# Performance work log

Measured on AMD Instinct MI355X. Metric: run time of the kernel, lower is better.

## Reference

```python
import jax, jax.numpy as jnp
import numpy as np

NORM_EPS = 1e-6
QK_SCALE = 1.0 / 128.0  # 1/d_head (muP)
ROTARY_BASE = 10000
INFTY_APPROX = 1e30

B, T, M, H, D = 2, 2048, 1024, 8, 128


def _rmsnorm(x, eps=NORM_EPS):
    # normalize over the last (head) dim; no learned gains (norm_gains=False)
    ms = jnp.mean(jnp.square(x), axis=-1, keepdims=True)
    return x / jnp.sqrt(ms + eps)


def _rope(x, base=ROTARY_BASE):
    # x: [b, h, t, d]; rotate (even-half, odd-half) pairs as in the source
    length, width = x.shape[-2], x.shape[-1]
    half = width // 2
    pos = jnp.arange(length, dtype=x.dtype)[:, None]            # [t, 1]
    freqs = jnp.power(jnp.asarray(base, x.dtype), -jnp.arange(half, dtype=x.dtype) / half)[None, :]
    rad = pos * freqs                                            # [t, half]
    cos = jnp.cos(rad)[None, None]
    sin = jnp.sin(rad)[None, None]
    even, odd = jnp.split(x, 2, axis=-1)
    return jnp.concatenate([even * cos - odd * sin, even * sin + odd * cos], axis=-1)


def setup_inputs() -> dict:
    key = jax.random.key(0)
    ks = jax.random.split(key, 5)
    std = M ** -0.5
    return {
        "x": jax.random.normal(ks[0], (B, T, M), jnp.float32),
        "wq": jax.random.normal(ks[1], (M, H, D), jnp.float32) * std,
        "wk": jax.random.normal(ks[2], (M, H, D), jnp.float32) * std,
        "wv": jax.random.normal(ks[3], (M, H, D), jnp.float32) * std,
        "wo": jax.random.normal(ks[4], (H, D, M), jnp.float32) * std,
    }


def reference(x, wq, wk, wv, wo):
    # projections: [b, h, t, d]
    q = jnp.einsum('bim,mhd->bhid', x, wq)
    k = jnp.einsum('bim,mhd->bhid', x, wk)
    v = jnp.einsum('bim,mhd->bhid', x, wv)
    # qk RMSNorm (norm_gains=False)
    q = _rmsnorm(q)
    k = _rmsnorm(k)
    # inline RoPE
    q = _rope(q)
    k = _rope(k)
    # scaled scores: mult applied to both q and k (mult^2 = qk_scale)
    mult = jnp.asarray(QK_SCALE ** 0.5, q.dtype)
    s = jnp.einsum('bhid,bhjd->bhij', q * mult, k * mult)
    # causal mask: subtract large constant where i < j
    t = s.shape[-1]
    mask = (jnp.arange(t)[:, None] < jnp.arange(t)[None, :]).astype(s.dtype)
    s = s - jnp.asarray(INFTY_APPROX, s.dtype) * mask[None, None]
    p = jax.nn.softmax(s, axis=-1)
    o = jnp.einsum('bhij,bhjd->bhid', p, v)
    return jnp.einsum('bhid,hdm->bim', o, wo)
```

## Files before the change

### kernel.cpp

```cpp
#include <hip/hip_runtime.h>
#include <hip/hip_bf16.h>
#include <math.h>

#define B_  2
#define T_  2048
#define M_  1024
#define H_  8
#define D_  128
#define NROW (B_ * T_)
#define HD  (H_ * D_)

#define NORM_EPS 1e-6f
#define QK_MULT  0.08838834764831845f
#define LN_BASE_64 0.14391156510f

typedef short bf16x8  __attribute__((ext_vector_type(8)));
typedef float f32x4   __attribute__((ext_vector_type(4)));
typedef float f32x16  __attribute__((ext_vector_type(16)));
typedef unsigned int uint32x2 __attribute__((ext_vector_type(2)));

static __device__ __forceinline__ unsigned short f2bf(float f) {
    union { __hip_bfloat16 h; unsigned short u; } cv;
    cv.h = __float2bfloat16(f);
    return cv.u;
}
static __device__ __forceinline__ unsigned int pk2bf(float a, float b) {
    return ((unsigned int)f2bf(b) << 16) | f2bf(a);
}

static __device__ __forceinline__ void gload_lds16(const unsigned short* g,
                                                   unsigned short* l) {
    __builtin_amdgcn_global_load_lds(
        (const __attribute__((address_space(1))) void*)g,
        (__attribute__((address_space(3))) void*)l, 16, 0, 0);
}

__global__ __launch_bounds__(256) void prep(const float* __restrict__ x,
                                            const float* __restrict__ w0,
                                            const float* __restrict__ w1,
                                            const float* __restrict__ w2,
                                            const float* __restrict__ w3,
                                            unsigned short* __restrict__ xb,
                                            unsigned short* __restrict__ wqkvT,
                                            unsigned short* __restrict__ woT,
                                            int* __restrict__ ctr)
{
    __shared__ float t[32][33];
    const int z = blockIdx.z;
    if (z == 4) {
        if (blockIdx.x == 0 && blockIdx.y == 0 && threadIdx.x < 8)
            ctr[threadIdx.x] = 0;
        const size_t base = ((size_t)blockIdx.y * 32 + blockIdx.x) * 4096;
        #pragma unroll
        for (int it = 0; it < 4; ++it) {
            const size_t i = base + it * 1024 + threadIdx.x * 4;
            const float4 v = *(const float4*)(x + i);
            ushort4 o;
            o.x = f2bf(v.x); o.y = f2bf(v.y); o.z = f2bf(v.z); o.w = f2bf(v.w);
            *(ushort4*)(xb + i) = o;
        }
        return;
    }
    const float* in = z == 0 ? w0 : (z == 1 ? w1 : (z == 2 ? w2 : w3));
    unsigned short* out = z < 3 ? (wqkvT + (size_t)z * 1024 * 1024) : woT;

    const int tx = threadIdx.x & 31;
    const int ty = threadIdx.x >> 5;
    const int n0 = blockIdx.x * 32;
    const int k0 = blockIdx.y * 32;
    #pragma unroll
    for (int r = 0; r < 4; ++r)
        t[ty + r * 8][tx] = in[(size_t)(k0 + ty + r * 8) * 1024 + n0 + tx];
    __syncthreads();
    #pragma unroll
    for (int r = 0; r < 4; ++r)
        out[(size_t)(n0 + ty + r * 8) * 1024 + k0 + tx] = f2bf(t[tx][ty + r * 8]);
}

__global__ __launch_bounds__(256) void gemm_qkv(const unsigned short* __restrict__ A,
                                                const unsigned short* __restrict__ Bt,
                                                unsigned short* __restrict__ oq,
                                                unsigned short* __restrict__ ok,
                                                unsigned short* __restrict__ vt)
{
    __shared__ __align__(16) unsigned short smem[17408];
    #define AsQ(buf) (smem + (buf) * 4096)
    #define BsQ(buf) (smem + 8192 + (buf) * 4096)

    const int tid  = threadIdx.x;
    const int lane = tid & 63;
    const int w    = tid >> 6;
    const int g    = lane >> 4;
    const int lc   = lane & 15;

    const int m0 = blockIdx.y * 128;
    const int n0 = blockIdx.x * 128;

    const unsigned short* aBase = A  + (size_t)m0 * 1024;
    const unsigned short* bBase = Bt + (size_t)n0 * 1024;

    int dstOff[2];
    size_t srcOff[2];
    #pragma unroll
    for (int it = 0; it < 2; ++it) {
        const int u  = tid + it * 256;
        const int r2 = u >> 2;
        const int sg = (u & 3) ^ (r2 & 3);
        dstOff[it] = u * 8;
        srcOff[it] = (size_t)r2 * 1024 + sg * 8;
    }

    f32x4 acc[2][8];
    #pragma unroll
    for (int i = 0; i < 2; ++i)
        #pragma unroll
        for (int j = 0; j < 8; ++j)
            acc[i][j] = (f32x4){0.f, 0.f, 0.f, 0.f};

    #pragma unroll
    for (int it = 0; it < 2; ++it) {
        gload_lds16(aBase + srcOff[it], AsQ(0) + dstOff[it]);
        gload_lds16(bBase + srcOff[it], BsQ(0) + dstOff[it]);
    }

    for (int kt = 0; kt < 32; ++kt) {
        const int cur = kt & 1;
        __syncthreads();

        if (kt < 31) {
            const int k0n = (kt + 1) * 32;
            #pragma unroll
            for (int it = 0; it < 2; ++it) {
                gload_lds16(aBase + srcOff[it] + k0n, AsQ(cur ^ 1) + dstOff[it]);
                gload_lds16(bBase + srcOff[it] + k0n, BsQ(cur ^ 1) + dstOff[it]);
            }
        }

        const int sw = (g ^ (lc & 3)) << 3;
        bf16x8 af[2], bfr[8];
        #pragma unroll
        for (int i = 0; i < 2; ++i)
            af[i] = *(const bf16x8*)&AsQ(cur)[(w * 32 + i * 16 + lc) * 32 + sw];
        #pragma unroll
        for (int j = 0; j < 8; ++j)
            bfr[j] = *(const bf16x8*)&BsQ(cur)[(j * 16 + lc) * 32 + sw];

        #pragma unroll
        for (int i = 0; i < 2; ++i)
            #pragma unroll
            for (int j = 0; j < 8; ++j)
                acc[i][j] = __builtin_amdgcn_mfma_f32_16x16x32_bf16(af[i], bfr[j], acc[i][j], 0, 0, 0);
    }

    const int which = n0 >> 10;
    const int ncol0 = n0 & 1023;
    if (which < 2) {
        unsigned short* outp = which == 0 ? oq : ok;
        float freq[4];
        #pragma unroll
        for (int j = 0; j < 4; ++j)
            freq[j] = __expf(-(float)(j * 16 + lc) * LN_BASE_64);

        #pragma unroll
        for (int i = 0; i < 2; ++i)
            #pragma unroll
            for (int r = 0; r < 4; ++r) {
                float s = 0.f;
                #pragma unroll
                for (int j = 0; j < 8; ++j) s += acc[i][j][r] * acc[i][j][r];
                #pragma unroll
                for (int off = 1; off < 16; off <<= 1) s += __shfl_xor(s, off);
                const float rms = rsqrtf(s * (1.0f / 128.0f) + NORM_EPS) * QK_MULT;

                const int trow = m0 + w * 32 + i * 16 + g * 4 + r;
                const float tpos = (float)(trow & (T_ - 1));
                unsigned short* op = outp + (size_t)trow * 1024 + ncol0;
                #pragma unroll
                for (int j = 0; j < 4; ++j) {
                    float sn, cs;
                    __sincosf(tpos * freq[j], &sn, &cs);
                    const float e = acc[i][j][r] * rms;
                    const float o = acc[i][j + 4][r] * rms;
                    op[j * 16 + lc]      = f2bf(e * cs - o * sn);
                    op[j * 16 + lc + 64] = f2bf(e * sn + o * cs);
                }
            }
    } else {
        const int b2 = m0 >> 11;
        const int hh = ncol0 >> 7;
        const int PAD = 136;
        __syncthreads();
        #pragma unroll
        for (int i = 0; i < 2; ++i) {
            const int t0 = w * 32 + i * 16 + g * 4;
            #pragma unroll
            for (int j = 0; j < 8; ++j) {
                uint2 val;
                val.x = pk2bf(acc[i][j][0], acc[i][j][1]);
                val.y = pk2bf(acc[i][j][2], acc[i][j][3]);
                *(uint2*)&smem[(j * 16 + lc) * PAD + t0] = val;
            }
        }
        __syncthreads();
        const int row  = tid >> 1;
        const int half = tid & 1;
        const unsigned short* src = &smem[row * PAD + half * 64];
        unsigned short* dst = vt + ((size_t)(b2 * 8 + hh) * 128 + row) * T_
                                 + (m0 & 2047) + half * 64;
        #pragma unroll
        for (int it2 = 0; it2 < 8; ++it2)
            *(uint4*)(dst + it2 * 8) = *(const uint4*)(src + it2 * 8);
    }
    #undef AsQ
    #undef BsQ
}

__global__ __launch_bounds__(256) void gemm_out(const unsigned short* __restrict__ A,
                                                const unsigned short* __restrict__ Bt,
                                                float* __restrict__ cf)
{
    __shared__ unsigned short As[2][128 * 64];
    __shared__ unsigned short Bs[2][64 * 64];

    const int tid  = threadIdx.x;
    const int lane = tid & 63;
    const int w    = tid >> 6;
    const int g    = lane >> 4;
    const int lc   = lane & 15;
    const int wm   = w >> 1;
    const int wn   = w & 1;

    const int m0 = blockIdx.y * 128;
    const int n0 = blockIdx.x * 64;

    const unsigned short* aBase = A  + (size_t)m0 * 1024;
    const unsigned short* bBase = Bt + (size_t)n0 * 1024;

    int dstA[4], dstB[2];
    size_t srcA[4], srcB[2];
    #pragma unroll
    for (int it = 0; it < 4; ++it) {
        const int u  = tid + it * 256;
        const int r2 = u >> 3;
        const int sg = (u & 7) ^ (r2 & 7);
        dstA[it] = u * 8;
        srcA[it] = (size_t)r2 * 1024 + sg * 8;
    }
    #pragma unroll
    for (int it = 0; it < 2; ++it) {
        const int u  = tid + it * 256;
        const int r2 = u >> 3;
        const int sg = (u & 7) ^ (r2 & 7);
        dstB[it] = u * 8;
        srcB[it] = (size_t)r2 * 1024 + sg * 8;
    }

    f32x4 acc[4][2];
    #pragma unroll
    for (int i = 0; i < 4; ++i)
        #pragma unroll
        for (int j = 0; j < 2; ++j)
            acc[i][j] = (f32x4){0.f, 0.f, 0.f, 0.f};

    #pragma unroll
    for (int it = 0; it < 4; ++it)
        gload_lds16(aBase + srcA[it], &As[0][dstA[it]]);
    #pragma unroll
    for (int it = 0; it < 2; ++it)
        gload_lds16(bBase + srcB[it], &Bs[0][dstB[it]]);

    for (int kt = 0; kt < 16; ++kt) {
        const int cur = kt & 1;
        __syncthreads();

        if (kt < 15) {
            const int k0n = (kt + 1) * 64;
            #pragma unroll
            for (int it = 0; it < 4; ++it)
                gload_lds16(aBase + srcA[it] + k0n, &As[cur ^ 1][dstA[it]]);
            #pragma unroll
            for (int it = 0; it < 2; ++it)
                gload_lds16(bBase + srcB[it] + k0n, &Bs[cur ^ 1][dstB[it]]);
        }

        #pragma unroll
        for (int dc = 0; dc < 2; ++dc) {
            const int sw = ((dc * 4 + g) ^ (lc & 7)) << 3;
            bf16x8 af[4], bfr[2];
            #pragma unroll
            for (int i = 0; i < 4; ++i)
                af[i] = *(const bf16x8*)&As[cur][(wm * 64 + i * 16 + lc) * 64 + sw];
            #pragma unroll
            for (int j = 0; j < 2; ++j)
                bfr[j] = *(const bf16x8*)&Bs[cur][(wn * 32 + j * 16 + lc) * 64 + sw];

            #pragma unroll
            for (int i = 0; i < 4; ++i)
                #pragma unroll
                for (int j = 0; j < 2; ++j)
                    acc[i][j] = __builtin_amdgcn_mfma_f32_16x16x32_bf16(af[i], bfr[j], acc[i][j], 0, 0, 0);
        }
    }

    #pragma unroll
    for (int i = 0; i < 4; ++i) {
        const int mrow = m0 + wm * 64 + i * 16 + g * 4;
        #pragma unroll
        for (int j = 0; j < 2; ++j) {
            const int nc = n0 + wn * 32 + j * 16 + lc;
            #pragma unroll
            for (int r = 0; r < 4; ++r)
                cf[(size_t)(mrow + r) * 1024 + nc] = acc[i][j][r];
        }
    }
}

__global__ __launch_bounds__(256) void flash_attn(const unsigned short* __restrict__ qb,
                                                  const unsigned short* __restrict__ kb,
                                                  const unsigned short* __restrict__ vt,
                                                  unsigned short* __restrict__ o,
                                                  int* __restrict__ ctr)
{
    __shared__ __align__(16) unsigned short smem[2 * 64 * 128 + 2 * 128 * 64 + 128];
    __shared__ int unitLds;
    unsigned short* KsB = smem;
    unsigned short* VsB = smem + 2 * 64 * 128;
    float* lscr = (float*)(smem + 2 * 64 * 128 + 2 * 128 * 64);
    float* scr  = (float*)smem;

    const int tid  = threadIdx.x;
    const int lane = tid & 63;
    const int w    = tid >> 6;
    const int wj   = w >> 1;
    const int wq2  = w & 1;
    const int qcol = lane & 31;
    const int hi   = lane >> 5;

    const int p = blockIdx.x & 7;

    int mI[4];
    size_t srcKoff[4], srcVoff[4];
    #pragma unroll
    for (int it = 0; it < 4; ++it) {
        const int m = (w * 4 + it) * 64 + lane;
        mI[it] = m;
        const int jK = m >> 4, cK = (m & 15) ^ (jK & 15);
        srcKoff[it] = (size_t)jK * 1024 + cK * 8;
        const int dV = m >> 3, cV = (m & 7) ^ (dV & 7);
        srcVoff[it] = (size_t)dV * T_ + cV * 8;
    }

    for (;;) {
        if (tid == 0) unitLds = atomicAdd(&ctr[p], 1);
        __syncthreads();
        const int u = unitLds;
        if (u >= 64) break;
        const int qt = 31 - (u >> 1);
        const int bh = p + 8 * (u & 1);
        const int q0 = qt * 64;
        const int h  = bh & (H_ - 1);
        const int b  = bh >> 3;

        const size_t bhbase  = (size_t)b * T_ * HD + (size_t)h * 128;
        const size_t bhvbase = (size_t)bh * 128 * T_;
        const unsigned short* kgb = kb + bhbase;
        const unsigned short* vgb = vt + bhvbase;

        bf16x8 qf[8];
        {
            const unsigned short* qp = qb + bhbase + (size_t)(q0 + wq2 * 32 + qcol) * 1024 + hi * 8;
            #pragma unroll
            for (int ks = 0; ks < 8; ++ks)
                qf[ks] = *(const bf16x8*)(qp + ks * 16);
        }

        float lsum = 0.f;
        f32x16 otacc[4];
        #pragma unroll
        for (int dch = 0; dch < 4; ++dch)
            #pragma unroll
            for (int r = 0; r < 16; ++r) otacc[dch][r] = 0.f;

        #pragma unroll
        for (int it = 0; it < 4; ++it) {
            gload_lds16(kgb + srcKoff[it], &KsB[mI[it] * 8]);
            gload_lds16(vgb + srcVoff[it], &VsB[mI[it] * 8]);
        }

        for (int jt = 0; jt <= qt; ++jt) {
            const int cur = jt & 1;
            unsigned short* Ks = KsB + cur * (64 * 128);
            unsigned short* Vs = VsB + cur * (128 * 64);
            __syncthreads();

            if (jt < qt) {
                const size_t j0n = (size_t)(jt + 1) * 64;
                unsigned short* Kn = KsB + (cur ^ 1) * (64 * 128);
                unsigned short* Vn = VsB + (cur ^ 1) * (128 * 64);
                #pragma unroll
                for (int it = 0; it < 4; ++it) {
                    gload_lds16(kgb + j0n * 1024 + srcKoff[it], &Kn[mI[it] * 8]);
                    gload_lds16(vgb + j0n + srcVoff[it], &Vn[mI[it] * 8]);
                }
            }

            const bool dead = (jt == qt) && (wj > wq2);
            if (!dead) {
                const int jrow = wj * 32 + qcol;

                bf16x8 kf[8], vf[8];
                #pragma unroll
                for (int ks = 0; ks < 8; ++ks) {
                    const int c = ks * 2 + hi;
                    kf[ks] = *(const bf16x8*)&Ks[(jrow * 16 + (c ^ (lane & 15))) * 8];
                }
                #pragma unroll
                for (int ks2 = 0; ks2 < 2; ++ks2)
                    #pragma unroll
                    for (int dch = 0; dch < 4; ++dch) {
                        const int c = wj * 4 + ks2 * 2 + hi;
                        const int drow = dch * 32 + qcol;
                        vf[ks2 * 4 + dch] = *(const bf16x8*)&Vs[(drow * 8 + (c ^ (lane & 7))) * 8];
                    }

                f32x16 sacc0, sacc1;
                #pragma unroll
                for (int r = 0; r < 16; ++r) { sacc0[r] = 0.f; sacc1[r] = 0.f; }
                __builtin_amdgcn_s_setprio(1);
                #pragma unroll
                for (int ks = 0; ks < 8; ks += 2) {
                    sacc0 = __builtin_amdgcn_mfma_f32_32x32x16_bf16(kf[ks], qf[ks], sacc0, 0, 0, 0);
                    sacc1 = __builtin_amdgcn_mfma_f32_32x32x16_bf16(kf[ks + 1], qf[ks + 1], sacc1, 0, 0, 0);
                }
                __builtin_amdgcn_s_setprio(0);
                f32x16 sacc = sacc0 + sacc1;

                if (jt == qt && wj == wq2) {
                    #pragma unroll
                    for (int r = 0; r < 16; ++r) {
                        const int jl = (r & 3) + 8 * (r >> 2) + 4 * hi;
                        if (qcol < jl) sacc[r] = -1e30f;
                    }
                }

                unsigned int dw[8];
                #pragma unroll
                for (int m2 = 0; m2 < 8; ++m2) {
                    const float p0 = __expf(sacc[2 * m2]);
                    const float p1 = __expf(sacc[2 * m2 + 1]);
                    lsum += p0 + p1;
                    dw[m2] = pk2bf(p0, p1);
                }

                __builtin_amdgcn_s_setprio(1);
                #pragma unroll
                for (int ks2 = 0; ks2 < 2; ++ks2) {
                    const uint32x2 s02 = __builtin_amdgcn_permlane32_swap(
                        dw[4 * ks2 + 0], dw[4 * ks2 + 2], 0, 0);
                    const uint32x2 s13 = __builtin_amdgcn_permlane32_swap(
                        dw[4 * ks2 + 1], dw[4 * ks2 + 3], 0, 0);
                    union { unsigned int u2[4]; bf16x8 v; } pf;
                    pf.u2[0] = s02[0];
                    pf.u2[1] = s13[0];
                    pf.u2[2] = s02[1];
                    pf.u2[3] = s13[1];
                    #pragma unroll
                    for (int dch = 0; dch < 4; ++dch)
                        otacc[dch] = __builtin_amdgcn_mfma_f32_32x32x16_bf16(vf[ks2 * 4 + dch], pf.v, otacc[dch], 0, 0, 0);
                }
                __builtin_amdgcn_s_setprio(0);
            }
        }

        lsum += __shfl_xor(lsum, 32);
        __syncthreads();

        if (wj == 1) {
            float* s0 = scr + (size_t)(wq2 * 32 + qcol) * 129;
            #pragma unroll
            for (int dch = 0; dch < 4; ++dch)
                #pragma unroll
                for (int r = 0; r < 16; ++r)
                    s0[dch * 32 + (r & 3) + 8 * (r >> 2) + 4 * hi] = otacc[dch][r];
            if (hi == 0) lscr[wq2 * 32 + qcol] = lsum;
        }
        __syncthreads();
        if (wj == 0) {
            const float l = lsum + lscr[wq2 * 32 + qcol];
            const float inv = 1.0f / l;
            const float* s0 = scr + (size_t)(wq2 * 32 + qcol) * 129;
            unsigned short* op = o + bhbase + (size_t)(q0 + wq2 * 32 + qcol) * 1024;
            #pragma unroll
            for (int dch = 0; dch < 4; ++dch) {
                #pragma unroll
                for (int k4 = 0; k4 < 4; ++k4) {
                    const int d0 = dch * 32 + 8 * k4 + 4 * hi;
                    const float f0 = (otacc[dch][4 * k4 + 0] + s0[d0 + 0]) * inv;
                    const float f1 = (otacc[dch][4 * k4 + 1] + s0[d0 + 1]) * inv;
                    const float f2 = (otacc[dch][4 * k4 + 2] + s0[d0 + 2]) * inv;
                    const float f3 = (otacc[dch][4 * k4 + 3] + s0[d0 + 3]) * inv;
                    uint2 val;
                    val.x = pk2bf(f0, f1);
                    val.y = pk2bf(f2, f3);
                    *(uint2*)(op + d0) = val;
                }
            }
        }
        __syncthreads();
    }
}

extern "C" void kernel_launch(void* const* d_in, const int* in_sizes, int n_in,
                              void* d_out, int out_size, void* d_ws, size_t ws_size,
                              hipStream_t stream)
{
    const float* x  = (const float*)d_in[0];
    const float* wq = (const float*)d_in[1];
    const float* wk = (const float*)d_in[2];
    const float* wv = (const float*)d_in[3];
    const float* wo = (const float*)d_in[4];
    float* out = (float*)d_out;

    const size_t SZ = (size_t)NROW * HD;
    unsigned short* qb    = (unsigned short*)d_ws;
    unsigned short* kb    = qb + SZ;
    unsigned short* vt    = kb + SZ;
    unsigned short* ob    = vt + SZ;
    unsigned short* xb    = ob + SZ;
    unsigned short* wqkvT = xb + SZ;
    unsigned short* woT   = wqkvT + 3 * 1024 * 1024;
    int* ctr = (int*)out;

    prep<<<dim3(32, 32, 5), 256, 0, stream>>>(x, wq, wk, wv, wo, xb, wqkvT, woT, ctr);

    gemm_qkv<<<dim3(24, 32), 256, 0, stream>>>(xb, wqkvT, qb, kb, vt);

    flash_attn<<<dim3(512), 256, 0, stream>>>(qb, kb, vt, ob, ctr);

    gemm_out<<<dim3(16, 32), 256, 0, stream>>>(ob, woT, out);
}
```

Baseline: 193.1 us.

## Split long causal query tiles across two blocks and merge partial outputs

Replaces the persistent atomic work-queue scheduling in flash attention with a static 48x16 grid. The 16 longest query tiles per head get two blocks, each covering half of the KV range. The first finisher writes unnormalized fp32 partial output and row sums to a scratch buffer (reusing the xb region), and the second spins on a per-tile counter, adds the partials and normalizes. This is meant to shorten the critical path of the longest causal tiles and improve load balance, at the cost of extra global traffic, a spin-wait that assumes both halves are co-resident, and more blocks overall.

```diff
diff --git a/kernel.cpp b/kernel.cpp
--- a/kernel.cpp
+++ b/kernel.cpp
@@ -43,13 +43,13 @@
                                             unsigned short* __restrict__ xb,
                                             unsigned short* __restrict__ wqkvT,
                                             unsigned short* __restrict__ woT,
-                                            int* __restrict__ ctr)
+                                            int* __restrict__ tctr)
 {
     __shared__ float t[32][33];
     const int z = blockIdx.z;
     if (z == 4) {
-        if (blockIdx.x == 0 && blockIdx.y == 0 && threadIdx.x < 8)
-            ctr[threadIdx.x] = 0;
+        if (blockIdx.x == 0 && blockIdx.y == 0)
+            tctr[threadIdx.x] = 0;
         const size_t base = ((size_t)blockIdx.y * 32 + blockIdx.x) * 4096;
         #pragma unroll
         for (int it = 0; it < 4; ++it) {
@@ -319,10 +319,12 @@
                                                   const unsigned short* __restrict__ kb,
                                                   const unsigned short* __restrict__ vt,
                                                   unsigned short* __restrict__ o,
-                                                  int* __restrict__ ctr)
+                                                  float* __restrict__ opart,
+                                                  float* __restrict__ lpart,
+                                                  int* __restrict__ tctr)
 {
     __shared__ __align__(16) unsigned short smem[2 * 64 * 128 + 2 * 128 * 64 + 128];
-    __shared__ int unitLds;
+    __shared__ int oldLds;
     unsigned short* KsB = smem;
     unsigned short* VsB = smem + 2 * 64 * 128;
     float* lscr = (float*)(smem + 2 * 64 * 128 + 2 * 128 * 64);
@@ -336,7 +338,25 @@
     const int qcol = lane & 31;
     const int hi   = lane >> 5;
 
-    const int p = blockIdx.x & 7;
+    const int x  = blockIdx.x;
+    const int bh = blockIdx.y;
+    int qt, jlo, jhi;
+    bool split;
+    if (x < 32) {
+        qt = 31 - (x & 15);
+        const int hsp = (qt + 2) >> 1;
+        split = true;
+        if (x < 16) { jlo = 0;   jhi = hsp - 1; }
+        else        { jlo = hsp; jhi = qt; }
+    } else {
+        qt = 47 - x; jlo = 0; jhi = qt; split = false;
+    }
+    const int q0 = qt * 64;
+    const int h  = bh & (H_ - 1);
+    const int b  = bh >> 3;
+
+    const size_t bhbase  = (size_t)b * T_ * HD + (size_t)h * 128;
+    const size_t bhvbase = (size_t)bh * 128 * T_;
 
     int mI[4];
     size_t srcKoff[4], srcVoff[4];
@@ -349,147 +369,141 @@
         const int dV = m >> 3, cV = (m & 7) ^ (dV & 7);
         srcVoff[it] = (size_t)dV * T_ + cV * 8;
     }
-
-    for (;;) {
-        if (tid == 0) unitLds = atomicAdd(&ctr[p], 1);
+    const unsigned short* kgb = kb + bhbase;
+    const unsigned short* vgb = vt + bhvbase;
+
+    bf16x8 qf[8];
+    {
+        const unsigned short* qp = qb + bhbase + (size_t)(q0 + wq2 * 32 + qcol) * 1024 + hi * 8;
+        #pragma unroll
+        for (int ks = 0; ks < 8; ++ks)
+            qf[ks] = *(const bf16x8*)(qp + ks * 16);
+    }
+
+    float lsum = 0.f;
+    f32x16 otacc[4];
+    #pragma unroll
+    for (int dch = 0; dch < 4; ++dch)
+        #pragma unroll
+        for (int r = 0; r < 16; ++r) otacc[dch][r] = 0.f;
+
+    {
+        const size_t j00 = (size_t)jlo * 64;
+        #pragma unroll
+        for (int it = 0; it < 4; ++it) {
+            gload_lds16(kgb + j00 * 1024 + srcKoff[it], &KsB[mI[it] * 8]);
+            gload_lds16(vgb + j00 + srcVoff[it], &VsB[mI[it] * 8]);
+        }
+    }
+
+    for (int jt = jlo; jt <= jhi; ++jt) {
+        const int cur = (jt - jlo) & 1;
+        unsigned short* Ks = KsB + cur * (64 * 128);
+        unsigned short* Vs = VsB + cur * (128 * 64);
         __syncthreads();
-        const int u = unitLds;
-        if (u >= 64) break;
-        const int qt = 31 - (u >> 1);
-        const int bh = p + 8 * (u & 1);
-        const int q0 = qt * 64;
-        const int h  = bh & (H_ - 1);
-        const int b  = bh >> 3;
-
-        const size_t bhbase  = (size_t)b * T_ * HD + (size_t)h * 128;
-        const size_t bhvbase = (size_t)bh * 128 * T_;
-        const unsigned short* kgb = kb + bhbase;
-        const unsigned short* vgb = vt + bhvbase;
-
-        bf16x8 qf[8];
-        {
-            const unsigned short* qp = qb + bhbase + (size_t)(q0 + wq2 * 32 + qcol) * 1024 + hi * 8;
-            #pragma unroll
-            for (int ks = 0; ks < 8; ++ks)
-                qf[ks] = *(const bf16x8*)(qp + ks * 16);
-        }
-
-        float lsum = 0.f;
-        f32x16 otacc[4];
+
+        if (jt < jhi) {
+            const size_t j0n = (size_t)(jt + 1) * 64;
+            unsigned short* Kn = KsB + (cur ^ 1) * (64 * 128);
+            unsigned short* Vn = VsB + (cur ^ 1) * (128 * 64);
+            #pragma unroll
+            for (int it = 0; it < 4; ++it) {
+                gload_lds16(kgb + j0n * 1024 + srcKoff[it], &Kn[mI[it] * 8]);
+                gload_lds16(vgb + j0n + srcVoff[it], &Vn[mI[it] * 8]);
+            }
+        }
+
+        const bool dead = (jt == qt) && (wj > wq2);
+        if (!dead) {
+            const int jrow = wj * 32 + qcol;
+
+            bf16x8 kf[8], vf[8];
+            #pragma unroll
+            for (int ks = 0; ks < 8; ++ks) {
+                const int c = ks * 2 + hi;
+                kf[ks] = *(const bf16x8*)&Ks[(jrow * 16 + (c ^ (lane & 15))) * 8];
+            }
+            #pragma unroll
+            for (int ks2 = 0; ks2 < 2; ++ks2)
+                #pragma unroll
+                for (int dch = 0; dch < 4; ++dch) {
+                    const int c = wj * 4 + ks2 * 2 + hi;
+                    const int drow = dch * 32 + qcol;
+                    vf[ks2 * 4 + dch] = *(const bf16x8*)&Vs[(drow * 8 + (c ^ (lane & 7))) * 8];
+                }
+
+            f32x16 sacc0, sacc1;
+            #pragma unroll
+            for (int r = 0; r < 16; ++r) { sacc0[r] = 0.f; sacc1[r] = 0.f; }
+            __builtin_amdgcn_s_setprio(1);
+            #pragma unroll
+            for (int ks = 0; ks < 8; ks += 2) {
+                sacc0 = __builtin_amdgcn_mfma_f32_32x32x16_bf16(kf[ks], qf[ks], sacc0, 0, 0, 0);
+                sacc1 = __builtin_amdgcn_mfma_f32_32x32x16_bf16(kf[ks + 1], qf[ks + 1], sacc1, 0, 0, 0);
+            }
+            __builtin_amdgcn_s_setprio(0);
+            f32x16 sacc = sacc0 + sacc1;
+
+            if (jt == qt && wj == wq2) {
+                #pragma unroll
+                for (int r = 0; r < 16; ++r) {
+                    const int jl = (r & 3) + 8 * (r >> 2) + 4 * hi;
+                    if (qcol < jl) sacc[r] = -1e30f;
+                }
+            }
+
+            unsigned int dw[8];
+            #pragma unroll
+            for (int m2 = 0; m2 < 8; ++m2) {
+                const float p0 = __expf(sacc[2 * m2]);
+                const float p1 = __expf(sacc[2 * m2 + 1]);
+                lsum += p0 + p1;
+                dw[m2] = pk2bf(p0, p1);
+            }
+
+            __builtin_amdgcn_s_setprio(1);
+            #pragma unroll
+            for (int ks2 = 0; ks2 < 2; ++ks2) {
+                const uint32x2 s02 = __builtin_amdgcn_permlane32_swap(
+                    dw[4 * ks2 + 0], dw[4 * ks2 + 2], 0, 0);
+                const uint32x2 s13 = __builtin_amdgcn_permlane32_swap(
+                    dw[4 * ks2 + 1], dw[4 * ks2 + 3], 0, 0);
+                union { unsigned int u2[4]; bf16x8 v; } pf;
+                pf.u2[0] = s02[0];
+                pf.u2[1] = s13[0];
+                pf.u2[2] = s02[1];
+                pf.u2[3] = s13[1];
+                #pragma unroll
+                for (int dch = 0; dch < 4; ++dch)
+                    otacc[dch] = __builtin_amdgcn_mfma_f32_32x32x16_bf16(vf[ks2 * 4 + dch], pf.v, otacc[dch], 0, 0, 0);
+            }
+            __builtin_amdgcn_s_setprio(0);
+        }
+    }
+
+    lsum += __shfl_xor(lsum, 32);
+    __syncthreads();
+
+    if (wj == 1) {
+        float* s0 = scr + (size_t)(wq2 * 32 + qcol) * 129;
         #pragma unroll
         for (int dch = 0; dch < 4; ++dch)
             #pragma unroll
-            for (int r = 0; r < 16; ++r) otacc[dch][r] = 0.f;
-
-        #pragma unroll
-        for (int it = 0; it < 4; ++it) {
-            gload_lds16(kgb + srcKoff[it], &KsB[mI[it] * 8]);
-            gload_lds16(vgb + srcVoff[it], &VsB[mI[it] * 8]);
-        }
-
-        for (int jt = 0; jt <= qt; ++jt) {
-            const int cur = jt & 1;
-            unsigned short* Ks = KsB + cur * (64 * 128);
-            unsigned short* Vs = VsB + cur * (128 * 64);
-            __syncthreads();
-
-            if (jt < qt) {
-                const size_t j0n = (size_t)(jt + 1) * 64;
-                unsigned short* Kn = KsB + (cur ^ 1) * (64 * 128);
-                unsigned short* Vn = VsB + (cur ^ 1) * (128 * 64);
-                #pragma unroll
-                for (int it = 0; it < 4; ++it) {
-                    gload_lds16(kgb + j0n * 1024 + srcKoff[it], &Kn[mI[it] * 8]);
-                    gload_lds16(vgb + j0n + srcVoff[it], &Vn[mI[it] * 8]);
-                }
-            }
-
-            const bool dead = (jt == qt) && (wj > wq2);
-            if (!dead) {
-                const int jrow = wj * 32 + qcol;
-
-                bf16x8 kf[8], vf[8];
-                #pragma unroll
-                for (int ks = 0; ks < 8; ++ks) {
-                    const int c = ks * 2 + hi;
-                    kf[ks] = *(const bf16x8*)&Ks[(jrow * 16 + (c ^ (lane & 15))) * 8];
-                }
-                #pragma unroll
-                for (int ks2 = 0; ks2 < 2; ++ks2)
-                    #pragma unroll
-                    for (int dch = 0; dch < 4; ++dch) {
-                        const int c = wj * 4 + ks2 * 2 + hi;
-                        const int drow = dch * 32 + qcol;
-                        vf[ks2 * 4 + dch] = *(const bf16x8*)&Vs[(drow * 8 + (c ^ (lane & 7))) * 8];
-                    }
-
-                f32x16 sacc0, sacc1;
-                #pragma unroll
-                for (int r = 0; r < 16; ++r) { sacc0[r] = 0.f; sacc1[r] = 0.f; }
-                __builtin_amdgcn_s_setprio(1);
-                #pragma unroll
-                for (int ks = 0; ks < 8; ks += 2) {
-                    sacc0 = __builtin_amdgcn_mfma_f32_32x32x16_bf16(kf[ks], qf[ks], sacc0, 0, 0, 0);
-                    sacc1 = __builtin_amdgcn_mfma_f32_32x32x16_bf16(kf[ks + 1], qf[ks + 1], sacc1, 0, 0, 0);
-                }
-                __builtin_amdgcn_s_setprio(0);
-                f32x16 sacc = sacc0 + sacc1;
-
-                if (jt == qt && wj == wq2) {
-                    #pragma unroll
-                    for (int r = 0; r < 16; ++r) {
-                        const int jl = (r & 3) + 8 * (r >> 2) + 4 * hi;
-                        if (qcol < jl) sacc[r] = -1e30f;
-                    }
-                }
-
-                unsigned int dw[8];
-                #pragma unroll
-                for (int m2 = 0; m2 < 8; ++m2) {
-                    const float p0 = __expf(sacc[2 * m2]);
-                    const float p1 = __expf(sacc[2 * m2 + 1]);
-                    lsum += p0 + p1;
-                    dw[m2] = pk2bf(p0, p1);
-                }
-
-                __builtin_amdgcn_s_setprio(1);
-                #pragma unroll
-                for (int ks2 = 0; ks2 < 2; ++ks2) {
-                    const uint32x2 s02 = __builtin_amdgcn_permlane32_swap(
-                        dw[4 * ks2 + 0], dw[4 * ks2 + 2], 0, 0);
-                    const uint32x2 s13 = __builtin_amdgcn_permlane32_swap(
-                        dw[4 * ks2 + 1], dw[4 * ks2 + 3], 0, 0);
-                    union { unsigned int u2[4]; bf16x8 v; } pf;
-                    pf.u2[0] = s02[0];
-                    pf.u2[1] = s13[0];
-                    pf.u2[2] = s02[1];
-                    pf.u2[3] = s13[1];
-                    #pragma unroll
-                    for (int dch = 0; dch < 4; ++dch)
-                        otacc[dch] = __builtin_amdgcn_mfma_f32_32x32x16_bf16(vf[ks2 * 4 + dch], pf.v, otacc[dch], 0, 0, 0);
-                }
-                __builtin_amdgcn_s_setprio(0);
-            }
-        }
-
-        lsum += __shfl_xor(lsum, 32);
-        __syncthreads();
-
-        if (wj == 1) {
-            float* s0 = scr + (size_t)(wq2 * 32 + qcol) * 129;
-            #pragma unroll
-            for (int dch = 0; dch < 4; ++dch)
-                #pragma unroll
-                for (int r = 0; r < 16; ++r)
-                    s0[dch * 32 + (r & 3) + 8 * (r >> 2) + 4 * hi] = otacc[dch][r];
-            if (hi == 0) lscr[wq2 * 32 + qcol] = lsum;
-        }
-        __syncthreads();
+            for (int r = 0; r < 16; ++r)
+                s0[dch * 32 + (r & 3) + 8 * (r >> 2) + 4 * hi] = otacc[dch][r];
+        if (hi == 0) lscr[wq2 * 32 + qcol] = lsum;
+    }
+    __syncthreads();
+
+    const int row = wq2 * 32 + qcol;
+    const float* s0 = scr + (size_t)row * 129;
+    float l = 0.f;
+    if (wj == 0) l = lsum + lscr[row];
+
+    if (!split) {
         if (wj == 0) {
-            const float l = lsum + lscr[wq2 * 32 + qcol];
             const float inv = 1.0f / l;
-            const float* s0 = scr + (size_t)(wq2 * 32 + qcol) * 129;
-            unsigned short* op = o + bhbase + (size_t)(q0 + wq2 * 32 + qcol) * 1024;
+            unsigned short* op = o + bhbase + (size_t)(q0 + row) * 1024;
             #pragma unroll
             for (int dch = 0; dch < 4; ++dch) {
                 #pragma unroll
@@ -506,7 +520,62 @@
                 }
             }
         }
+    } else {
+        const int tidx = bh * 16 + (qt - 16);
+        float* po = opart + (size_t)tidx * (64 * 128);
+
+        if (tid == 0) oldLds = atomicAdd(&tctr[tidx], 1);
         __syncthreads();
+
+        if (oldLds == 0) {
+            if (wj == 0) {
+                float* pr = po + row * 128;
+                #pragma unroll
+                for (int dch = 0; dch < 4; ++dch)
+                    #pragma unroll
+                    for (int k4 = 0; k4 < 4; ++k4) {
+                        const int d0 = dch * 32 + 8 * k4 + 4 * hi;
+                        float4 v;
+                        v.x = otacc[dch][4 * k4 + 0] + s0[d0 + 0];
+                        v.y = otacc[dch][4 * k4 + 1] + s0[d0 + 1];
+                        v.z = otacc[dch][4 * k4 + 2] + s0[d0 + 2];
+                        v.w = otacc[dch][4 * k4 + 3] + s0[d0 + 3];
+                        *(float4*)(pr + d0) = v;
+                    }
+                if (hi == 0) lpart[tidx * 64 + row] = l;
+            }
+            __threadfence();
+            __syncthreads();
+            if (tid == 0) atomicAdd(&tctr[tidx], 1);
+        } else {
+            if (tid == 0) {
+                while (atomicAdd(&tctr[tidx], 0) < 3)
+                    __builtin_amdgcn_s_sleep(16);
+            }
+            __syncthreads();
+            __threadfence();
+            if (wj == 0) {
+                const float inv = 1.0f / (l + lpart[tidx * 64 + row]);
+                const float* pr = po + row * 128;
+                unsigned short* op = o + bhbase + (size_t)(q0 + row) * 1024;
+                #pragma unroll
+                for (int dch = 0; dch < 4; ++dch) {
+                    #pragma unroll
+                    for (int k4 = 0; k4 < 4; ++k4) {
+                        const int d0 = dch * 32 + 8 * k4 + 4 * hi;
+                        const float4 pv = *(const float4*)(pr + d0);
+                        const float f0 = (otacc[dch][4 * k4 + 0] + s0[d0 + 0] + pv.x) * inv;
+                        const float f1 = (otacc[dch][4 * k4 + 1] + s0[d0 + 1] + pv.y) * inv;
+                        const float f2 = (otacc[dch][4 * k4 + 2] + s0[d0 + 2] + pv.z) * inv;
+                        const float f3 = (otacc[dch][4 * k4 + 3] + s0[d0 + 3] + pv.w) * inv;
+                        uint2 val;
+                        val.x = pk2bf(f0, f1);
+                        val.y = pk2bf(f2, f3);
+                        *(uint2*)(op + d0) = val;
+                    }
+                }
+            }
+        }
     }
 }
 
@@ -529,13 +598,16 @@
     unsigned short* xb    = ob + SZ;
     unsigned short* wqkvT = xb + SZ;
     unsigned short* woT   = wqkvT + 3 * 1024 * 1024;
-    int* ctr = (int*)out;
-
-    prep<<<dim3(32, 32, 5), 256, 0, stream>>>(x, wq, wk, wv, wo, xb, wqkvT, woT, ctr);
+
+    float* opart = (float*)xb;
+    float* lpart = (float*)wqkvT;
+    int*   tctr  = (int*)out;
+
+    prep<<<dim3(32, 32, 5), 256, 0, stream>>>(x, wq, wk, wv, wo, xb, wqkvT, woT, tctr);
 
     gemm_qkv<<<dim3(24, 32), 256, 0, stream>>>(xb, wqkvT, qb, kb, vt);
 
-    flash_attn<<<dim3(512), 256, 0, stream>>>(qb, kb, vt, ob, ctr);
+    flash_attn<<<dim3(48, 16), 256, 0, stream>>>(qb, kb, vt, ob, opart, lpart, tctr);
 
     gemm_out<<<dim3(16, 32), 256, 0, stream>>>(ob, woT, out);
 }
```

Result: slower. 278.4 us (+44.2%).

## Replace persistent atomic-scheduled attention with static 128-row blocks and triple buffering

Applied to the files above, without the earlier changes.

The attention kernel drops the persistent work queue driven by an atomic counter and instead launches one 512-thread block per 128-query tile and head pair on a 16x16 grid. K/V tiles are staged into a three-deep LDS ring with explicit vmcnt waits and raw barriers, so loads run two tiles ahead. The counter reset in prep is removed. Larger blocks reuse each staged K/V tile across twice as many query rows, but static scheduling may load-balance the causal triangle worse and uses more LDS per block, which can lower occupancy.

```diff
diff --git a/kernel.cpp b/kernel.cpp
--- a/kernel.cpp
+++ b/kernel.cpp
@@ -42,14 +42,11 @@
                                             const float* __restrict__ w3,
                                             unsigned short* __restrict__ xb,
                                             unsigned short* __restrict__ wqkvT,
-                                            unsigned short* __restrict__ woT,
-                                            int* __restrict__ ctr)
+                                            unsigned short* __restrict__ woT)
 {
     __shared__ float t[32][33];
     const int z = blockIdx.z;
     if (z == 4) {
-        if (blockIdx.x == 0 && blockIdx.y == 0 && threadIdx.x < 8)
-            ctr[threadIdx.x] = 0;
         const size_t base = ((size_t)blockIdx.y * 32 + blockIdx.x) * 4096;
         #pragma unroll
         for (int it = 0; it < 4; ++it) {
@@ -315,198 +312,192 @@
     }
 }
 
-__global__ __launch_bounds__(256) void flash_attn(const unsigned short* __restrict__ qb,
+__global__ __launch_bounds__(512) void flash_attn(const unsigned short* __restrict__ qb,
                                                   const unsigned short* __restrict__ kb,
                                                   const unsigned short* __restrict__ vt,
-                                                  unsigned short* __restrict__ o,
-                                                  int* __restrict__ ctr)
+                                                  unsigned short* __restrict__ o)
 {
-    __shared__ __align__(16) unsigned short smem[2 * 64 * 128 + 2 * 128 * 64 + 128];
-    __shared__ int unitLds;
-    unsigned short* KsB = smem;
-    unsigned short* VsB = smem + 2 * 64 * 128;
-    float* lscr = (float*)(smem + 2 * 64 * 128 + 2 * 128 * 64);
+    __shared__ __align__(16) unsigned short smem[6 * 8192 + 256];
+    unsigned short* K3 = smem;
+    unsigned short* V3 = smem + 3 * 8192;
+    float* lscr = (float*)(smem + 6 * 8192);
     float* scr  = (float*)smem;
 
     const int tid  = threadIdx.x;
     const int lane = tid & 63;
     const int w    = tid >> 6;
-    const int wj   = w >> 1;
-    const int wq2  = w & 1;
+    const int qg   = w & 3;
+    const int wj   = w >> 2;
     const int qcol = lane & 31;
     const int hi   = lane >> 5;
 
-    const int p = blockIdx.x & 7;
-
-    int mI[4];
-    size_t srcKoff[4], srcVoff[4];
-    #pragma unroll
-    for (int it = 0; it < 4; ++it) {
-        const int m = (w * 4 + it) * 64 + lane;
-        mI[it] = m;
+    const int qbk = blockIdx.x;
+    const int bh  = blockIdx.y;
+    const int jmax = 2 * qbk + 1;
+    const int q0  = qbk * 128;
+    const int h   = bh & (H_ - 1);
+    const int b   = bh >> 3;
+
+    const size_t bhbase  = (size_t)b * T_ * HD + (size_t)h * 128;
+    const size_t bhvbase = (size_t)bh * 128 * T_;
+
+    int mK[2], mV[2];
+    size_t srcK[2], srcV[2];
+    #pragma unroll
+    for (int it = 0; it < 2; ++it) {
+        const int m = tid + it * 512;
+        mK[it] = m;
         const int jK = m >> 4, cK = (m & 15) ^ (jK & 15);
-        srcKoff[it] = (size_t)jK * 1024 + cK * 8;
+        srcK[it] = (size_t)jK * 1024 + cK * 8;
+        mV[it] = m;
         const int dV = m >> 3, cV = (m & 7) ^ (dV & 7);
-        srcVoff[it] = (size_t)dV * T_ + cV * 8;
-    }
-
-    for (;;) {
-        if (tid == 0) unitLds = atomicAdd(&ctr[p], 1);
-        __syncthreads();
-        const int u = unitLds;
-        if (u >= 64) break;
-        const int qt = 31 - (u >> 1);
-        const int bh = p + 8 * (u & 1);
-        const int q0 = qt * 64;
-        const int h  = bh & (H_ - 1);
-        const int b  = bh >> 3;
-
-        const size_t bhbase  = (size_t)b * T_ * HD + (size_t)h * 128;
-        const size_t bhvbase = (size_t)bh * 128 * T_;
-        const unsigned short* kgb = kb + bhbase;
-        const unsigned short* vgb = vt + bhvbase;
-
-        bf16x8 qf[8];
-        {
-            const unsigned short* qp = qb + bhbase + (size_t)(q0 + wq2 * 32 + qcol) * 1024 + hi * 8;
-            #pragma unroll
-            for (int ks = 0; ks < 8; ++ks)
-                qf[ks] = *(const bf16x8*)(qp + ks * 16);
-        }
-
-        float lsum = 0.f;
-        f32x16 otacc[4];
+        srcV[it] = (size_t)dV * T_ + cV * 8;
+    }
+    const unsigned short* kgb = kb + bhbase;
+    const unsigned short* vgb = vt + bhvbase;
+
+#define STAGE(jt_, b_) {                                                     \
+        const size_t jo = (size_t)(jt_) * 64;                                \
+        unsigned short* Kd = K3 + (b_) * 8192;                               \
+        unsigned short* Vd = V3 + (b_) * 8192;                               \
+        _Pragma("unroll")                                                    \
+        for (int it = 0; it < 2; ++it)                                       \
+            gload_lds16(kgb + jo * 1024 + srcK[it], &Kd[mK[it] * 8]);        \
+        _Pragma("unroll")                                                    \
+        for (int it = 0; it < 2; ++it)                                       \
+            gload_lds16(vgb + jo + srcV[it], &Vd[mV[it] * 8]);               \
+    }
+
+    bf16x8 qf[8];
+    {
+        const unsigned short* qp = qb + bhbase + (size_t)(q0 + qg * 32 + qcol) * 1024 + hi * 8;
+        #pragma unroll
+        for (int ks = 0; ks < 8; ++ks)
+            qf[ks] = *(const bf16x8*)(qp + ks * 16);
+    }
+
+    float lsum = 0.f;
+    f32x16 otacc[4];
+    #pragma unroll
+    for (int dch = 0; dch < 4; ++dch)
+        #pragma unroll
+        for (int r = 0; r < 16; ++r) otacc[dch][r] = 0.f;
+
+    STAGE(0, 0);
+    STAGE(1, 1);
+
+    for (int jt = 0; jt <= jmax; ++jt) {
+        if (jt < jmax) asm volatile("s_waitcnt vmcnt(4)" ::: "memory");
+        else           asm volatile("s_waitcnt vmcnt(0)" ::: "memory");
+        __builtin_amdgcn_s_barrier();
+        if (jt + 2 <= jmax) STAGE(jt + 2, (jt + 2) % 3);
+
+        unsigned short* Ks = K3 + (jt % 3) * 8192;
+        unsigned short* Vs = V3 + (jt % 3) * 8192;
+
+        const int e = qg - 2 * (jt - 2 * qbk) - wj;
+        if (e >= 0) {
+            const int jrow = wj * 32 + qcol;
+
+            bf16x8 kf[8], vf[8];
+            #pragma unroll
+            for (int ks = 0; ks < 8; ++ks) {
+                const int c = ks * 2 + hi;
+                kf[ks] = *(const bf16x8*)&Ks[(jrow * 16 + (c ^ (lane & 15))) * 8];
+            }
+            #pragma unroll
+            for (int ks2 = 0; ks2 < 2; ++ks2)
+                #pragma unroll
+                for (int dch = 0; dch < 4; ++dch) {
+                    const int c = wj * 4 + ks2 * 2 + hi;
+                    const int drow = dch * 32 + qcol;
+                    vf[ks2 * 4 + dch] = *(const bf16x8*)&Vs[(drow * 8 + (c ^ (lane & 7))) * 8];
+                }
+
+            f32x16 sacc0, sacc1;
+            #pragma unroll
+            for (int r = 0; r < 16; ++r) { sacc0[r] = 0.f; sacc1[r] = 0.f; }
+            __builtin_amdgcn_s_setprio(1);
+            #pragma unroll
+            for (int ks = 0; ks < 8; ks += 2) {
+                sacc0 = __builtin_amdgcn_mfma_f32_32x32x16_bf16(kf[ks], qf[ks], sacc0, 0, 0, 0);
+                sacc1 = __builtin_amdgcn_mfma_f32_32x32x16_bf16(kf[ks + 1], qf[ks + 1], sacc1, 0, 0, 0);
+            }
+            __builtin_amdgcn_s_setprio(0);
+            f32x16 sacc = sacc0 + sacc1;
+
+            if (e == 0) {
+                #pragma unroll
+                for (int r = 0; r < 16; ++r) {
+                    const int jl = (r & 3) + 8 * (r >> 2) + 4 * hi;
+                    if (qcol < jl) sacc[r] = -1e30f;
+                }
+            }
+
+            unsigned int dw[8];
+            #pragma unroll
+            for (int m2 = 0; m2 < 8; ++m2) {
+                const float p0 = __expf(sacc[2 * m2]);
+                const float p1 = __expf(sacc[2 * m2 + 1]);
+                lsum += p0 + p1;
+                dw[m2] = pk2bf(p0, p1);
+            }
+
+            __builtin_amdgcn_s_setprio(1);
+            #pragma unroll
+            for (int ks2 = 0; ks2 < 2; ++ks2) {
+                const uint32x2 s02 = __builtin_amdgcn_permlane32_swap(
+                    dw[4 * ks2 + 0], dw[4 * ks2 + 2], 0, 0);
+                const uint32x2 s13 = __builtin_amdgcn_permlane32_swap(
+                    dw[4 * ks2 + 1], dw[4 * ks2 + 3], 0, 0);
+                union { unsigned int u2[4]; bf16x8 v; } pf;
+                pf.u2[0] = s02[0];
+                pf.u2[1] = s13[0];
+                pf.u2[2] = s02[1];
+                pf.u2[3] = s13[1];
+                #pragma unroll
+                for (int dch = 0; dch < 4; ++dch)
+                    otacc[dch] = __builtin_amdgcn_mfma_f32_32x32x16_bf16(vf[ks2 * 4 + dch], pf.v, otacc[dch], 0, 0, 0);
+            }
+            __builtin_amdgcn_s_setprio(0);
+        }
+    }
+#undef STAGE
+
+    lsum += __shfl_xor(lsum, 32);
+    __syncthreads();
+
+    const int row = qg * 32 + qcol;
+    if (wj == 1) {
+        float* s0 = scr + (size_t)row * 129;
         #pragma unroll
         for (int dch = 0; dch < 4; ++dch)
             #pragma unroll
-            for (int r = 0; r < 16; ++r) otacc[dch][r] = 0.f;
-
-        #pragma unroll
-        for (int it = 0; it < 4; ++it) {
-            gload_lds16(kgb + srcKoff[it], &KsB[mI[it] * 8]);
-            gload_lds16(vgb + srcVoff[it], &VsB[mI[it] * 8]);
-        }
-
-        for (int jt = 0; jt <= qt; ++jt) {
-            const int cur = jt & 1;
-            unsigned short* Ks = KsB + cur * (64 * 128);
-            unsigned short* Vs = VsB + cur * (128 * 64);
-            __syncthreads();
-
-            if (jt < qt) {
-                const size_t j0n = (size_t)(jt + 1) * 64;
-                unsigned short* Kn = KsB + (cur ^ 1) * (64 * 128);
-                unsigned short* Vn = VsB + (cur ^ 1) * (128 * 64);
-                #pragma unroll
-                for (int it = 0; it < 4; ++it) {
-                    gload_lds16(kgb + j0n * 1024 + srcKoff[it], &Kn[mI[it] * 8]);
-                    gload_lds16(vgb + j0n + srcVoff[it], &Vn[mI[it] * 8]);
-                }
-            }
-
-            const bool dead = (jt == qt) && (wj > wq2);
-            if (!dead) {
-                const int jrow = wj * 32 + qcol;
-
-                bf16x8 kf[8], vf[8];
-                #pragma unroll
-                for (int ks = 0; ks < 8; ++ks) {
-                    const int c = ks * 2 + hi;
-                    kf[ks] = *(const bf16x8*)&Ks[(jrow * 16 + (c ^ (lane & 15))) * 8];
-                }
-                #pragma unroll
-                for (int ks2 = 0; ks2 < 2; ++ks2)
-                    #pragma unroll
-                    for (int dch = 0; dch < 4; ++dch) {
-                        const int c = wj * 4 + ks2 * 2 + hi;
-                        const int drow = dch * 32 + qcol;
-                        vf[ks2 * 4 + dch] = *(const bf16x8*)&Vs[(drow * 8 + (c ^ (lane & 7))) * 8];
-                    }
-
-                f32x16 sacc0, sacc1;
-                #pragma unroll
-                for (int r = 0; r < 16; ++r) { sacc0[r] = 0.f; sacc1[r] = 0.f; }
-                __builtin_amdgcn_s_setprio(1);
-                #pragma unroll
-                for (int ks = 0; ks < 8; ks += 2) {
-                    sacc0 = __builtin_amdgcn_mfma_f32_32x32x16_bf16(kf[ks], qf[ks], sacc0, 0, 0, 0);
-                    sacc1 = __builtin_amdgcn_mfma_f32_32x32x16_bf16(kf[ks + 1], qf[ks + 1], sacc1, 0, 0, 0);
-                }
-                __builtin_amdgcn_s_setprio(0);
-                f32x16 sacc = sacc0 + sacc1;
-
-                if (jt == qt && wj == wq2) {
-                    #pragma unroll
-                    for (int r = 0; r < 16; ++r) {
-                        const int jl = (r & 3) + 8 * (r >> 2) + 4 * hi;
-                        if (qcol < jl) sacc[r] = -1e30f;
-                    }
-                }
-
-                unsigned int dw[8];
-                #pragma unroll
-                for (int m2 = 0; m2 < 8; ++m2) {
-                    const float p0 = __expf(sacc[2 * m2]);
-                    const float p1 = __expf(sacc[2 * m2 + 1]);
-                    lsum += p0 + p1;
-                    dw[m2] = pk2bf(p0, p1);
-                }
-
-                __builtin_amdgcn_s_setprio(1);
-                #pragma unroll
-                for (int ks2 = 0; ks2 < 2; ++ks2) {
-                    const uint32x2 s02 = __builtin_amdgcn_permlane32_swap(
-                        dw[4 * ks2 + 0], dw[4 * ks2 + 2], 0, 0);
-                    const uint32x2 s13 = __builtin_amdgcn_permlane32_swap(
-                        dw[4 * ks2 + 1], dw[4 * ks2 + 3], 0, 0);
-                    union { unsigned int u2[4]; bf16x8 v; } pf;
-                    pf.u2[0] = s02[0];
-                    pf.u2[1] = s13[0];
-                    pf.u2[2] = s02[1];
-                    pf.u2[3] = s13[1];
-                    #pragma unroll
-                    for (int dch = 0; dch < 4; ++dch)
-                        otacc[dch] = __builtin_amdgcn_mfma_f32_32x32x16_bf16(vf[ks2 * 4 + dch], pf.v, otacc[dch], 0, 0, 0);
-                }
-                __builtin_amdgcn_s_setprio(0);
-            }
-        }
-
-        lsum += __shfl_xor(lsum, 32);
-        __syncthreads();
-
-        if (wj == 1) {
-            float* s0 = scr + (size_t)(wq2 * 32 + qcol) * 129;
-            #pragma unroll
-            for (int dch = 0; dch < 4; ++dch)
-                #pragma unroll
-                for (int r = 0; r < 16; ++r)
-                    s0[dch * 32 + (r & 3) + 8 * (r >> 2) + 4 * hi] = otacc[dch][r];
-            if (hi == 0) lscr[wq2 * 32 + qcol] = lsum;
-        }
-        __syncthreads();
-        if (wj == 0) {
-            const float l = lsum + lscr[wq2 * 32 + qcol];
-            const float inv = 1.0f / l;
-            const float* s0 = scr + (size_t)(wq2 * 32 + qcol) * 129;
-            unsigned short* op = o + bhbase + (size_t)(q0 + wq2 * 32 + qcol) * 1024;
-            #pragma unroll
-            for (int dch = 0; dch < 4; ++dch) {
-                #pragma unroll
-                for (int k4 = 0; k4 < 4; ++k4) {
-                    const int d0 = dch * 32 + 8 * k4 + 4 * hi;
-                    const float f0 = (otacc[dch][4 * k4 + 0] + s0[d0 + 0]) * inv;
-                    const float f1 = (otacc[dch][4 * k4 + 1] + s0[d0 + 1]) * inv;
-                    const float f2 = (otacc[dch][4 * k4 + 2] + s0[d0 + 2]) * inv;
-                    const float f3 = (otacc[dch][4 * k4 + 3] + s0[d0 + 3]) * inv;
-                    uint2 val;
-                    val.x = pk2bf(f0, f1);
-                    val.y = pk2bf(f2, f3);
-                    *(uint2*)(op + d0) = val;
-                }
-            }
-        }
-        __syncthreads();
+            for (int r = 0; r < 16; ++r)
+                s0[dch * 32 + (r & 3) + 8 * (r >> 2) + 4 * hi] = otacc[dch][r];
+        if (hi == 0) lscr[row] = lsum;
+    }
+    __syncthreads();
+    if (wj == 0) {
+        const float l = lsum + lscr[row];
+        const float inv = 1.0f / l;
+        const float* s0 = scr + (size_t)row * 129;
+        unsigned short* op = o + bhbase + (size_t)(q0 + row) * 1024;
+        #pragma unroll
+        for (int dch = 0; dch < 4; ++dch) {
+            #pragma unroll
+            for (int k4 = 0; k4 < 4; ++k4) {
+                const int d0 = dch * 32 + 8 * k4 + 4 * hi;
+                const float f0 = (otacc[dch][4 * k4 + 0] + s0[d0 + 0]) * inv;
+                const float f1 = (otacc[dch][4 * k4 + 1] + s0[d0 + 1]) * inv;
+                const float f2 = (otacc[dch][4 * k4 + 2] + s0[d0 + 2]) * inv;
+                const float f3 = (otacc[dch][4 * k4 + 3] + s0[d0 + 3]) * inv;
+                uint2 val;
+                val.x = pk2bf(f0, f1);
+                val.y = pk2bf(f2, f3);
+                *(uint2*)(op + d0) = val;
+            }
+        }
     }
 }
 
@@ -529,13 +520,12 @@
     unsigned short* xb    = ob + SZ;
     unsigned short* wqkvT = xb + SZ;
     unsigned short* woT   = wqkvT + 3 * 1024 * 1024;
-    int* ctr = (int*)out;
-
-    prep<<<dim3(32, 32, 5), 256, 0, stream>>>(x, wq, wk, wv, wo, xb, wqkvT, woT, ctr);
+
+    prep<<<dim3(32, 32, 5), 256, 0, stream>>>(x, wq, wk, wv, wo, xb, wqkvT, woT);
 
     gemm_qkv<<<dim3(24, 32), 256, 0, stream>>>(xb, wqkvT, qb, kb, vt);
 
-    flash_attn<<<dim3(512), 256, 0, stream>>>(qb, kb, vt, ob, ctr);
+    flash_attn<<<dim3(16, 16), 512, 0, stream>>>(qb, kb, vt, ob);
 
     gemm_out<<<dim3(16, 32), 256, 0, stream>>>(ob, woT, out);
 }
```

Result: faster. 187.6 us (-2.9%).
